# Kernel tuning notes

Hardware: AMD Instinct MI355X
Metric: run time of the kernel (lower is better)

Reference implementation:

```python
import jax, jax.numpy as jnp
import numpy as np
from jax import lax

STRIDE = (1, 1)
PADDING = ((1, 1), (1, 1))
DILATION = (1, 1)


def setup_inputs() -> dict:
    key = jax.random.key(0)
    k1, k2 = jax.random.split(key)
    input = jax.random.normal(k1, (32, 128, 56, 56), dtype=jnp.float32)
    weight = jax.random.normal(k2, (256, 128, 3, 3), dtype=jnp.float32)
    bias = jnp.zeros((256,), dtype=jnp.float32)
    return {"input": input, "weight": weight, "bias": bias}


def reference(input, weight, bias):
    # The original builds the conv's dense matrix via conv2d on an identity
    # basis and then matmuls; that is mathematically identical to a direct
    # conv2d (the map is linear), plus the broadcast bias.
    out = lax.conv_general_dilated(
        input, weight,
        window_strides=STRIDE,
        padding=PADDING,
        rhs_dilation=DILATION,
        dimension_numbers=("NCHW", "OIHW", "NCHW"),
    )
    return out + bias[None, :, None, None]
```

## Files before the change

kernel.cpp:

```cpp
#include <hip/hip_runtime.h>
#include <hip/hip_bf16.h>
#include <stdint.h>


typedef __attribute__((ext_vector_type(8))) short bf16x8;
typedef __attribute__((ext_vector_type(8))) unsigned short ushort8;
typedef __attribute__((ext_vector_type(4))) float f32x4;

#define HW       56
#define SPATIAL  3136
#define C_IN     128
#define K_OUT    256
#define GEMM_K   1152
#define GEMM_N   100352

#define PHW      58
#define PIMG     3364
#define PADTOT_AL 107656

#define BM       256
#define BN       128
#define NTILE    18
#define BUFH     24576

__device__ __forceinline__ unsigned short f2bf(float f) {
    union { float f; unsigned int u; } v; v.f = f;
    unsigned int u = v.u + 0x7FFFu + ((v.u >> 16) & 1u);
    return (unsigned short)(u >> 16);
}

__device__ __forceinline__ void gload16(const unsigned short* g, unsigned short* l) {
    __builtin_amdgcn_global_load_lds(
        (const __attribute__((address_space(1))) unsigned int*)(g),
        (__attribute__((address_space(3))) unsigned int*)(l),
        16, 0, 0);
}

__global__ __launch_bounds__(256)
void prep_kernel(const float* __restrict__ w, unsigned short* __restrict__ w3,
                 unsigned short* __restrict__ pad) {
    if (blockIdx.x < 1152) {
        int idx = blockIdx.x * 256 + threadIdx.x;
        int rc   = idx / 18432;
        int rem  = idx % 18432;
        int tap  = rem / 2048;
        int rem2 = rem % 2048;
        int cc   = rem2 / 512;
        int s    = rem2 % 512;
        int l    = s >> 3, j = s & 7;
        int ko   = rc * 16 + (l & 15);
        int c    = cc * 32 + ((l >> 4) << 3) + j;
        w3[idx] = f2bf(w[(ko * C_IN + c) * 9 + tap]);
    } else {
        int idx = (blockIdx.x - 1152) * 256 + threadIdx.x;
        if (idx >= 29184) return;
        int cc  = idx / 7296;
        int r   = idx % 7296;
        int img = r / 228;
        int p   = r % 228;
        int pos;
        if (p < 58)       pos = p;
        else if (p < 116) pos = 57 * PHW + (p - 58);
        else { int i = p - 116; pos = (1 + (i >> 1)) * PHW + (i & 1) * 57; }
        unsigned short* d = pad + (size_t)cc * PADTOT_AL * 32
                          + ((size_t)img * PIMG + pos) * 32;
        const ushort8 z = (ushort8){0,0,0,0,0,0,0,0};
        *reinterpret_cast<ushort8*>(d)      = z;
        *reinterpret_cast<ushort8*>(d + 8)  = z;
        *reinterpret_cast<ushort8*>(d + 16) = z;
        *reinterpret_cast<ushort8*>(d + 24) = z;
    }
}

__global__ __launch_bounds__(256)
void intrans_kernel(const float* __restrict__ in, unsigned short* __restrict__ pad) {
    __shared__ __attribute__((aligned(16))) unsigned short l[56 * 136];
    const int bx = blockIdx.x;
    const int n = bx / HW, h = bx % HW;
    const int tid = threadIdx.x;
    const float* src = in + (size_t)n * C_IN * SPATIAL + h * HW;
    #pragma unroll
    for (int i = 0; i < 28; ++i) {
        int idx = i * 256 + tid;
        int c = idx / HW, w = idx % HW;
        l[w * 136 + c] = f2bf(src[(size_t)c * SPATIAL + w]);
    }
    __syncthreads();
    const int prow = n * PIMG + (h + 1) * PHW;
    #pragma unroll
    for (int j = 0; j < 4; ++j) {
        int chunk = j * 256 + tid;
        if (chunk < 896) {
            int w = chunk >> 4, c8 = chunk & 15;
            int cc = c8 >> 2, sub = c8 & 3;
            unsigned short* dst = pad + (size_t)cc * PADTOT_AL * 32
                                + (size_t)(prow + w + 1) * 32 + sub * 8;
            *reinterpret_cast<ushort8*>(dst) =
                *reinterpret_cast<const ushort8*>(&l[w * 136 + c8 * 8]);
        }
    }
}

__global__ __launch_bounds__(512, 1)
void conv_pipe(const unsigned short* __restrict__ pad,
               const unsigned short* __restrict__ w3,
               const float* __restrict__ bias,
               float* __restrict__ out) {
    __shared__ __attribute__((aligned(16))) unsigned short lds[3 * BUFH];

    const int tid  = threadIdx.x;
    const int wave = tid >> 6;
    const int lane = tid & 63;
    const int la   = lane & 15;
    const int lkh  = lane >> 4;

    const int bid = blockIdx.x;
    const int nt  = (bid & 7) * 98 + (bid >> 3);
    const int g0  = nt * BN;

    const int wr = wave >> 1, wc = wave & 1;

    const unsigned short* aw0 = w3 + (size_t)(wave * 2 + 0) * 18432 + lane * 8;
    const unsigned short* aw1 = w3 + (size_t)(wave * 2 + 1) * 18432 + lane * 8;
    const unsigned short* bsrc;
    {
        int col = g0 + wave * 16 + la;
        int img = col / SPATIAL;
        int pos = col - img * SPATIAL;
        int oh  = pos / HW, ow = pos - oh * HW;
        bsrc = pad + (size_t)(img * PIMG + (oh + 1) * PHW + (ow + 1)) * 32 + lkh * 8;
    }

    f32x4 acc[4][4];
    #pragma unroll
    for (int i = 0; i < 4; ++i)
        #pragma unroll
        for (int j = 0; j < 4; ++j)
            acc[i][j] = (f32x4){0.f, 0.f, 0.f, 0.f};

    auto STAGE = [&](int tn, int kc) {
        const int tap = tn >> 1;
        const int cc  = (tn & 1) * 2 + kc;
        const int dr = tap / 3 - 1, dsx = tap % 3 - 1;
        unsigned short* dst = &lds[(tn % 3) * BUFH];
        gload16(aw0 + (size_t)(tap * 4 + cc) * 512, dst + (wave * 4 + kc) * 512);
        gload16(aw1 + (size_t)(tap * 4 + cc) * 512, dst + (wave * 4 + 2 + kc) * 512);
        gload16(bsrc + (size_t)cc * PADTOT_AL * 32 + (dr * PHW + dsx) * 32,
                dst + 16384 + (wave * 2 + kc) * 512);
    };

    bf16x8 a0[4], b0[4], a1[4], b1[4];

    auto READ0 = [&](int tn, int ks) {
        const unsigned short* Ab = &lds[(tn % 3) * BUFH];
        #pragma unroll
        for (int mi = 0; mi < 4; ++mi)
            a0[mi] = *reinterpret_cast<const bf16x8*>(
                &Ab[((wr * 4 + mi) * 2 + ks) * 512 + lane * 8]);
        #pragma unroll
        for (int nj = 0; nj < 4; ++nj)
            b0[nj] = *reinterpret_cast<const bf16x8*>(
                &Ab[16384 + ((wc * 4 + nj) * 2 + ks) * 512 + lane * 8]);
    };
    auto READ1 = [&](int tn, int ks) {
        const unsigned short* Ab = &lds[(tn % 3) * BUFH];
        #pragma unroll
        for (int mi = 0; mi < 4; ++mi)
            a1[mi] = *reinterpret_cast<const bf16x8*>(
                &Ab[((wr * 4 + mi) * 2 + ks) * 512 + lane * 8]);
        #pragma unroll
        for (int nj = 0; nj < 4; ++nj)
            b1[nj] = *reinterpret_cast<const bf16x8*>(
                &Ab[16384 + ((wc * 4 + nj) * 2 + ks) * 512 + lane * 8]);
    };

    STAGE(0, 0); STAGE(0, 1);
    STAGE(1, 0); STAGE(1, 1);
    asm volatile("s_waitcnt vmcnt(6)" ::: "memory");
    __builtin_amdgcn_s_barrier();
    asm volatile("" ::: "memory");
    READ0(0, 0);

    #pragma unroll
    for (int t = 0; t < NTILE; ++t) {
        READ1(t, 1);
        if (t + 2 < NTILE) STAGE(t + 2, 0);
        asm volatile("s_waitcnt lgkmcnt(8)" ::: "memory");
        __builtin_amdgcn_sched_barrier(0);
        __builtin_amdgcn_s_setprio(1);
        #pragma unroll
        for (int mi = 0; mi < 4; ++mi)
            #pragma unroll
            for (int nj = 0; nj < 4; ++nj)
                acc[mi][nj] = __builtin_amdgcn_mfma_f32_16x16x32_bf16(
                    a0[mi], b0[nj], acc[mi][nj], 0, 0, 0);
        __builtin_amdgcn_s_setprio(0);

        if (t + 2 < NTILE) STAGE(t + 2, 1);
        asm volatile("s_waitcnt lgkmcnt(0)" ::: "memory");
        __builtin_amdgcn_sched_barrier(0);
        if (t + 1 < NTILE) {
            if (t + 2 < NTILE)
                asm volatile("s_waitcnt vmcnt(6)" ::: "memory");
            else
                asm volatile("s_waitcnt vmcnt(0)" ::: "memory");
            __builtin_amdgcn_s_barrier();
            asm volatile("" ::: "memory");
            READ0(t + 1, 0);
        }
        __builtin_amdgcn_s_setprio(1);
        #pragma unroll
        for (int mi = 0; mi < 4; ++mi)
            #pragma unroll
            for (int nj = 0; nj < 4; ++nj)
                acc[mi][nj] = __builtin_amdgcn_mfma_f32_16x16x32_bf16(
                    a1[mi], b1[nj], acc[mi][nj], 0, 0, 0);
        __builtin_amdgcn_s_setprio(0);
    }

    #pragma unroll
    for (int mi = 0; mi < 4; ++mi) {
        const int mb = wr * 64 + mi * 16 + lkh * 4;
        const f32x4 bv4 = *reinterpret_cast<const f32x4*>(&bias[mb]);
        #pragma unroll
        for (int nj = 0; nj < 4; ++nj) {
            const int gcol = g0 + wc * 64 + nj * 16;
            const int n2 = gcol / SPATIAL;
            const int p2 = gcol - n2 * SPATIAL + la;
            float* op = out + ((size_t)(n2 * K_OUT + mb)) * SPATIAL + p2;
            op[0]                   = acc[mi][nj][0] + bv4[0];
            op[SPATIAL]             = acc[mi][nj][1] + bv4[1];
            op[2 * SPATIAL]         = acc[mi][nj][2] + bv4[2];
            op[3 * (size_t)SPATIAL] = acc[mi][nj][3] + bv4[3];
        }
    }
}

#define LDK 40
__global__ __launch_bounds__(256)
void conv_mfma_fallback(const float* __restrict__ in,
                        const float* __restrict__ wraw,
                        const float* __restrict__ bias,
                        float* __restrict__ out) {
    __shared__ __attribute__((aligned(16))) unsigned short lA[128 * LDK];
    __shared__ __attribute__((aligned(16))) unsigned short lB[128 * LDK];
    const int tid = threadIdx.x;
    const int m0  = blockIdx.y * 128;
    const int g0  = blockIdx.x * 128;
    const int wave = tid >> 6, lane = tid & 63;
    const int wr = wave >> 1, wc = wave & 1;
    const int la = lane & 15, lkh = lane >> 4, lk = lkh * 8;

    f32x4 acc[4][4];
    #pragma unroll
    for (int i = 0; i < 4; ++i)
        #pragma unroll
        for (int j = 0; j < 4; ++j)
            acc[i][j] = (f32x4){0.f, 0.f, 0.f, 0.f};

    const int jj = tid & 127;
    const int kb = (tid >> 7) * 16;
    const int g = g0 + jj;
    const int nimg = g / SPATIAL;
    const int pos  = g % SPATIAL;
    const int oh = pos / HW, ow = pos % HW;

    for (int tap = 0; tap < 9; ++tap) {
        const int dr = tap / 3 - 1, dsx = tap % 3 - 1;
        const int ih = oh + dr, iw = ow + dsx;
        const bool valid = ((unsigned)ih < HW) && ((unsigned)iw < HW);
        const float* src = in + ((nimg * C_IN) * HW + ih) * HW + iw;
        for (int c0 = 0; c0 < C_IN; c0 += 32) {
            #pragma unroll
            for (int i = 0; i < 2; ++i) {
                const int ch = tid * 2 + i;
                const int row = ch >> 2;
                const int kp = (ch & 3) * 8;
                ushort8 v;
                #pragma unroll
                for (int e = 0; e < 8; ++e)
                    v[e] = f2bf(wraw[((m0 + row) * C_IN + c0 + kp + e) * 9 + tap]);
                *reinterpret_cast<ushort8*>(&lA[row * LDK + kp]) = v;
            }
            {
                ushort8 v0, v1;
                #pragma unroll
                for (int i = 0; i < 8; ++i)
                    v0[i] = f2bf(valid ? src[(c0 + kb + i) * SPATIAL] : 0.f);
                #pragma unroll
                for (int i = 0; i < 8; ++i)
                    v1[i] = f2bf(valid ? src[(c0 + kb + 8 + i) * SPATIAL] : 0.f);
                *reinterpret_cast<ushort8*>(&lB[jj * LDK + kb])     = v0;
                *reinterpret_cast<ushort8*>(&lB[jj * LDK + kb + 8]) = v1;
            }
            __syncthreads();
            bf16x8 af[4], bv[4];
            #pragma unroll
            for (int f = 0; f < 4; ++f) {
                af[f] = *reinterpret_cast<const bf16x8*>(&lA[(wr * 64 + f * 16 + la) * LDK + lk]);
                bv[f] = *reinterpret_cast<const bf16x8*>(&lB[(wc * 64 + f * 16 + la) * LDK + lk]);
            }
            #pragma unroll
            for (int fi = 0; fi < 4; ++fi)
                #pragma unroll
                for (int fj = 0; fj < 4; ++fj)
                    acc[fi][fj] = __builtin_amdgcn_mfma_f32_16x16x32_bf16(
                        af[fi], bv[fj], acc[fi][fj], 0, 0, 0);
            __syncthreads();
        }
    }
    const int mbase = m0 + wr * 64;
    const int cbase = g0 + wc * 64;
    #pragma unroll
    for (int fi = 0; fi < 4; ++fi) {
        float bvv[4];
        #pragma unroll
        for (int r = 0; r < 4; ++r)
            bvv[r] = bias[mbase + fi * 16 + lkh * 4 + r];
        #pragma unroll
        for (int fj = 0; fj < 4; ++fj) {
            const int gcol = cbase + fj * 16 + la;
            const int n2 = gcol / SPATIAL;
            const int p2 = gcol % SPATIAL;
            float* op = out + (size_t)(n2 * K_OUT) * SPATIAL + p2;
            #pragma unroll
            for (int r = 0; r < 4; ++r)
                op[(size_t)(mbase + fi * 16 + lkh * 4 + r) * SPATIAL] = acc[fi][fj][r] + bvv[r];
        }
    }
}

extern "C" void kernel_launch(void* const* d_in, const int* in_sizes, int n_in,
                              void* d_out, int out_size, void* d_ws, size_t ws_size,
                              hipStream_t stream) {
    const float* in   = (const float*)d_in[0];
    const float* w    = (const float*)d_in[1];
    const float* bias = (const float*)d_in[2];
    float* out = (float*)d_out;

    const size_t pad_halves = 4ull * PADTOT_AL * 32ull;
    const size_t need_bytes = (pad_halves + 294912ull) * 2ull;

    if (ws_size >= need_bytes) {
        unsigned short* pad = (unsigned short*)d_ws;
        unsigned short* w3  = pad + pad_halves;
        prep_kernel<<<1152 + 114, 256, 0, stream>>>(w, w3, pad);
        intrans_kernel<<<32 * HW, 256, 0, stream>>>(in, pad);
        conv_pipe<<<GEMM_N / BN, 512, 0, stream>>>(pad, w3, bias, out);
    } else {
        dim3 grid(GEMM_N / 128, K_OUT / 128);
        conv_mfma_fallback<<<grid, 256, 0, stream>>>(in, w, bias, out);
    }
}
```

Baseline: 97.74 us.

## Split conv GEMM tile across 16 waves instead of 8

After: 96.67 us. No clear change (-1.1%).

```diff
diff --git a/kernel.cpp b/kernel.cpp
--- a/kernel.cpp
+++ b/kernel.cpp
@@ -101,11 +101,11 @@
     }
 }
 
-__global__ __launch_bounds__(512, 1)
-void conv_pipe(const unsigned short* __restrict__ pad,
-               const unsigned short* __restrict__ w3,
-               const float* __restrict__ bias,
-               float* __restrict__ out) {
+__global__ __launch_bounds__(1024, 1)
+void conv_tlp(const unsigned short* __restrict__ pad,
+              const unsigned short* __restrict__ w3,
+              const float* __restrict__ bias,
+              float* __restrict__ out) {
     __shared__ __attribute__((aligned(16))) unsigned short lds[3 * BUFH];
 
     const int tid  = threadIdx.x;
@@ -118,38 +118,44 @@
     const int nt  = (bid & 7) * 98 + (bid >> 3);
     const int g0  = nt * BN;
 
-    const int wr = wave >> 1, wc = wave & 1;
-
-    const unsigned short* aw0 = w3 + (size_t)(wave * 2 + 0) * 18432 + lane * 8;
-    const unsigned short* aw1 = w3 + (size_t)(wave * 2 + 1) * 18432 + lane * 8;
+    const int wr = wave >> 2, wc = wave & 3;
+
+    const unsigned short* aw = w3 + (size_t)wave * 18432 + lane * 8;
     const unsigned short* bsrc;
     {
-        int col = g0 + wave * 16 + la;
+        int col = g0 + (wave >> 1) * 16 + la;
         int img = col / SPATIAL;
         int pos = col - img * SPATIAL;
         int oh  = pos / HW, ow = pos - oh * HW;
         bsrc = pad + (size_t)(img * PIMG + (oh + 1) * PHW + (ow + 1)) * 32 + lkh * 8;
     }
-
-    f32x4 acc[4][4];
+    const int bkc = wave & 1;
+
+    f32x4 acc[4][2];
     #pragma unroll
     for (int i = 0; i < 4; ++i)
         #pragma unroll
-        for (int j = 0; j < 4; ++j)
+        for (int j = 0; j < 2; ++j)
             acc[i][j] = (f32x4){0.f, 0.f, 0.f, 0.f};
 
-    auto STAGE = [&](int tn, int kc) {
-        const int tap = tn >> 1;
-        const int cc  = (tn & 1) * 2 + kc;
+    auto STAGE_A0 = [&](int tn) {
+        const int tap = tn >> 1, cc = (tn & 1) * 2;
+        gload16(aw + (size_t)(tap * 4 + cc) * 512,
+                &lds[(tn % 3) * BUFH] + (wave * 2 + 0) * 512);
+    };
+    auto STAGE_A1 = [&](int tn) {
+        const int tap = tn >> 1, cc = (tn & 1) * 2 + 1;
+        gload16(aw + (size_t)(tap * 4 + cc) * 512,
+                &lds[(tn % 3) * BUFH] + (wave * 2 + 1) * 512);
+    };
+    auto STAGE_B = [&](int tn) {
+        const int tap = tn >> 1, cc = (tn & 1) * 2 + bkc;
         const int dr = tap / 3 - 1, dsx = tap % 3 - 1;
-        unsigned short* dst = &lds[(tn % 3) * BUFH];
-        gload16(aw0 + (size_t)(tap * 4 + cc) * 512, dst + (wave * 4 + kc) * 512);
-        gload16(aw1 + (size_t)(tap * 4 + cc) * 512, dst + (wave * 4 + 2 + kc) * 512);
-        gload16(bsrc + (size_t)cc * PADTOT_AL * 32 + (dr * PHW + dsx) * 32,
-                dst + 16384 + (wave * 2 + kc) * 512);
-    };
-
-    bf16x8 a0[4], b0[4], a1[4], b1[4];
+        gload16(bsrc + (size_t)cc * (PADTOT_AL * 32) + (dr * PHW + dsx) * 32,
+                &lds[(tn % 3) * BUFH] + 16384 + wave * 512);
+    };
+
+    bf16x8 a0[4], b0[2], a1[4], b1[2];
 
     auto READ0 = [&](int tn, int ks) {
         const unsigned short* Ab = &lds[(tn % 3) * BUFH];
@@ -158,9 +164,9 @@
             a0[mi] = *reinterpret_cast<const bf16x8*>(
                 &Ab[((wr * 4 + mi) * 2 + ks) * 512 + lane * 8]);
         #pragma unroll
-        for (int nj = 0; nj < 4; ++nj)
+        for (int nj = 0; nj < 2; ++nj)
             b0[nj] = *reinterpret_cast<const bf16x8*>(
-                &Ab[16384 + ((wc * 4 + nj) * 2 + ks) * 512 + lane * 8]);
+                &Ab[16384 + ((wc * 2 + nj) * 2 + ks) * 512 + lane * 8]);
     };
     auto READ1 = [&](int tn, int ks) {
         const unsigned short* Ab = &lds[(tn % 3) * BUFH];
@@ -169,14 +175,14 @@
             a1[mi] = *reinterpret_cast<const bf16x8*>(
                 &Ab[((wr * 4 + mi) * 2 + ks) * 512 + lane * 8]);
         #pragma unroll
-        for (int nj = 0; nj < 4; ++nj)
+        for (int nj = 0; nj < 2; ++nj)
             b1[nj] = *reinterpret_cast<const bf16x8*>(
-                &Ab[16384 + ((wc * 4 + nj) * 2 + ks) * 512 + lane * 8]);
-    };
-
-    STAGE(0, 0); STAGE(0, 1);
-    STAGE(1, 0); STAGE(1, 1);
-    asm volatile("s_waitcnt vmcnt(6)" ::: "memory");
+                &Ab[16384 + ((wc * 2 + nj) * 2 + ks) * 512 + lane * 8]);
+    };
+
+    STAGE_A0(0); STAGE_A1(0); STAGE_B(0);
+    STAGE_A0(1); STAGE_A1(1); STAGE_B(1);
+    asm volatile("s_waitcnt vmcnt(3)" ::: "memory");
     __builtin_amdgcn_s_barrier();
     asm volatile("" ::: "memory");
     READ0(0, 0);
@@ -184,24 +190,24 @@
     #pragma unroll
     for (int t = 0; t < NTILE; ++t) {
         READ1(t, 1);
-        if (t + 2 < NTILE) STAGE(t + 2, 0);
-        asm volatile("s_waitcnt lgkmcnt(8)" ::: "memory");
+        if (t + 2 < NTILE) { STAGE_A0(t + 2); STAGE_B(t + 2); }
+        asm volatile("s_waitcnt lgkmcnt(6)" ::: "memory");
         __builtin_amdgcn_sched_barrier(0);
         __builtin_amdgcn_s_setprio(1);
         #pragma unroll
         for (int mi = 0; mi < 4; ++mi)
             #pragma unroll
-            for (int nj = 0; nj < 4; ++nj)
+            for (int nj = 0; nj < 2; ++nj)
                 acc[mi][nj] = __builtin_amdgcn_mfma_f32_16x16x32_bf16(
                     a0[mi], b0[nj], acc[mi][nj], 0, 0, 0);
         __builtin_amdgcn_s_setprio(0);
 
-        if (t + 2 < NTILE) STAGE(t + 2, 1);
+        if (t + 2 < NTILE) STAGE_A1(t + 2);
         asm volatile("s_waitcnt lgkmcnt(0)" ::: "memory");
         __builtin_amdgcn_sched_barrier(0);
         if (t + 1 < NTILE) {
             if (t + 2 < NTILE)
-                asm volatile("s_waitcnt vmcnt(6)" ::: "memory");
+                asm volatile("s_waitcnt vmcnt(3)" ::: "memory");
             else
                 asm volatile("s_waitcnt vmcnt(0)" ::: "memory");
             __builtin_amdgcn_s_barrier();
@@ -212,7 +218,7 @@
         #pragma unroll
         for (int mi = 0; mi < 4; ++mi)
             #pragma unroll
-            for (int nj = 0; nj < 4; ++nj)
+            for (int nj = 0; nj < 2; ++nj)
                 acc[mi][nj] = __builtin_amdgcn_mfma_f32_16x16x32_bf16(
                     a1[mi], b1[nj], acc[mi][nj], 0, 0, 0);
         __builtin_amdgcn_s_setprio(0);
@@ -223,8 +229,8 @@
         const int mb = wr * 64 + mi * 16 + lkh * 4;
         const f32x4 bv4 = *reinterpret_cast<const f32x4*>(&bias[mb]);
         #pragma unroll
-        for (int nj = 0; nj < 4; ++nj) {
-            const int gcol = g0 + wc * 64 + nj * 16;
+        for (int nj = 0; nj < 2; ++nj) {
+            const int gcol = g0 + wc * 32 + nj * 16;
             const int n2 = gcol / SPATIAL;
             const int p2 = gcol - n2 * SPATIAL + la;
             float* op = out + ((size_t)(n2 * K_OUT + mb)) * SPATIAL + p2;
@@ -346,7 +352,7 @@
         unsigned short* w3  = pad + pad_halves;
         prep_kernel<<<1152 + 114, 256, 0, stream>>>(w, w3, pad);
         intrans_kernel<<<32 * HW, 256, 0, stream>>>(in, pad);
-        conv_pipe<<<GEMM_N / BN, 512, 0, stream>>>(pad, w3, bias, out);
+        conv_tlp<<<GEMM_N / BN, 1024, 0, stream>>>(pad, w3, bias, out);
     } else {
         dim3 grid(GEMM_N / 128, K_OUT / 128);
         conv_mfma_fallback<<<grid, 256, 0, stream>>>(in, w, bias, out);
```
